# Optimization experiments

Hardware: AMD Instinct MI355X
Metric: run time of the kernel (lower is better)

## Reference

```python
import jax, jax.numpy as jnp
import numpy as np

B, N, K = 2, 8192, 16
D1, D2, OUT = 128, 256, 128


def setup_inputs() -> dict:
    key = jax.random.key(0)
    ks = jax.random.split(key, 6)
    return {
        "xyz1": jax.random.normal(ks[0], (B, N, 3), dtype=jnp.float32),
        "xyz2": jax.random.normal(ks[1], (B, N, 3), dtype=jnp.float32),
        "points1": jax.random.normal(ks[2], (B, N, D1), dtype=jnp.float32),
        "points2": jax.random.normal(ks[3], (B, N, D2), dtype=jnp.float32),
        # Conv1d(k=1) == pointwise linear: weight [OUT, D1+D2], bias [OUT]
        "W": jax.random.normal(ks[4], (OUT, D1 + D2), dtype=jnp.float32) / np.sqrt(D1 + D2).astype(np.float32),
        "b": jax.random.normal(ks[5], (OUT,), dtype=jnp.float32) * 0.01,
        "nsample": K,
    }


def reference(xyz1, xyz2, points1, points2, W, b, nsample):
    Bb, Nn, _ = xyz1.shape
    # squared pairwise distances, queries=xyz2, keys=xyz1 -> [B, N, N]
    d2 = (jnp.sum(xyz2 * xyz2, -1)[:, :, None]
          + jnp.sum(xyz1 * xyz1, -1)[:, None, :]
          - 2.0 * jnp.einsum('bsc,bnc->bsn', xyz2, xyz1))
    neg_vals, idx = jax.lax.top_k(-d2, nsample)          # K nearest
    dists = -neg_vals                                     # [B, N, K] sq dists
    recip = 1.0 / (dists + 1e-8)
    weight = recip / jnp.sum(recip, axis=2, keepdims=True)  # inverse-dist weights
    # gather neighbor features from points2: [B, N, K, D2]
    g = jnp.take_along_axis(points2, idx.reshape(Bb, Nn * nsample)[:, :, None], axis=1)
    g = g.reshape(Bb, Nn, nsample, -1)
    interp = jnp.sum(g * weight[..., None], axis=2)       # [B, N, D2]
    cat = jnp.concatenate([points1, interp], axis=-1)     # [B, N, D1+D2]
    # Conv1d(kernel=1) over channel dim
    return jnp.einsum('bnc,oc->bno', cat, W) + b
```

## Files before the change

kernel.cpp:

```cpp
#include <hip/hip_runtime.h>
#include <stdint.h>

#define BQ   2
#define NQ   8192
#define D1Q  128
#define D2Q  256
#define OUTQ 128
#define CATQ 384
#define KQ   16

#define NBIN 4096
#define RED_MARGIN 1e-3f
#define LB_MARGIN  1e-2f

#define WREG 3152

#define WS_WFH   0
#define WS_WFL   98304
#define WS_SPXYZ 262144
#define WS_QSXYZ 524288
#define WS_SPIDX 786432
#define WS_QSIDX 819200
#define WS_GBLO  851968
#define WS_GBHI  856064

__device__ __forceinline__ ushort f2bf(float f) {
    uint32_t u = __float_as_uint(f);
    return (ushort)((u + 0x7FFFu + ((u >> 16) & 1u)) >> 16);
}
__device__ __forceinline__ float bf2f(ushort h) {
    return __uint_as_float((uint32_t)h << 16);
}

__device__ __forceinline__ uint32_t encf(float f) {
    uint32_t b = __float_as_uint(f);
    return b ^ (0x80000000u | (uint32_t)((int32_t)b >> 31));
}
__device__ __forceinline__ float decf(uint32_t u) {
    uint32_t bits = (u & 0x80000000u) ? (u ^ 0x80000000u) : ~u;
    return __uint_as_float(bits);
}

__device__ __forceinline__ uint32_t mbcnt64(uint64_t m) {
    return __builtin_amdgcn_mbcnt_hi((uint32_t)(m >> 32),
           __builtin_amdgcn_mbcnt_lo((uint32_t)m, 0u));
}

typedef __attribute__((ext_vector_type(8))) short short8v;
typedef __attribute__((ext_vector_type(4))) float f32x4v;

__device__ __forceinline__ int mort_bin(float x, float y, float z) {
    int bx = (int)((x + 5.0f) * 1.6f); bx = bx < 0 ? 0 : (bx > 15 ? 15 : bx);
    int by = (int)((y + 5.0f) * 1.6f); by = by < 0 ? 0 : (by > 15 ? 15 : by);
    int bz = (int)((z + 5.0f) * 1.6f); bz = bz < 0 ? 0 : (bz > 15 ? 15 : bz);
    int k = 0;
    #pragma unroll
    for (int t = 0; t < 4; ++t)
        k |= (((bx >> t) & 1) << (3 * t)) | (((by >> t) & 1) << (3 * t + 1)) |
             (((bz >> t) & 1) << (3 * t + 2));
    return k;
}

__global__ __launch_bounds__(1024) void prep_all_kernel(
        const float* __restrict__ W,
        ushort* __restrict__ Wfh, ushort* __restrict__ Wfl,
        const float* __restrict__ xyz1, const float* __restrict__ xyz2,
        float4* __restrict__ sp_xyzn, float4* __restrict__ qs_xyzw,
        ushort* __restrict__ sp_idx, ushort* __restrict__ qs_idx,
        float4* __restrict__ gblo, float4* __restrict__ gbhi) {
    __shared__ uint32_t hist[NBIN];
    __shared__ uint32_t sc[16];
    __shared__ uint32_t ab[128 * 8];

    const int bid = blockIdx.x;
    const int tid = threadIdx.x;

    if (bid >= 4) {
        int flat = (bid - 4) * 1024 + tid;
        if (flat < CATQ * OUTQ) {
            int r    = flat & 7;
            int lane = (flat >> 3) & 63;
            int ctk  = flat >> 9;
            int ct   = ctk & 7;
            int kt   = ctk >> 3;
            int o = ct * 16 + (lane & 15);
            int k = kt * 32 + (lane >> 4) * 8 + r;
            float v  = W[o * CATQ + k];
            ushort h = f2bf(v);
            Wfh[flat] = h;
            Wfl[flat] = f2bf(v - bf2f(h));
        }
        return;
    }

    const int  batch = bid & 1;
    const bool isPts = bid < 2;
    const float* src = (isPts ? xyz1 : xyz2) + (size_t)batch * NQ * 3;

    #pragma unroll
    for (int i = tid; i < NBIN; i += 1024) hist[i] = 0u;
    if (isPts) ab[tid] = ((tid & 7) >= 4) ? 0u : 0xFFFFFFFFu;
    __syncthreads();

    float x[8], y[8], z[8];
    int   bin[8];
    #pragma unroll
    for (int e = 0; e < 8; ++e) {
        int idx = e * 1024 + tid;
        const float* p = src + (size_t)idx * 3;
        x[e] = p[0]; y[e] = p[1]; z[e] = p[2];
        bin[e] = mort_bin(x[e], y[e], z[e]);
        atomicAdd(&hist[bin[e]], 1u);
    }
    __syncthreads();

    uint32_t v0 = hist[4 * tid], v1 = hist[4 * tid + 1],
             v2 = hist[4 * tid + 2], v3 = hist[4 * tid + 3];
    uint32_t s = v0 + v1 + v2 + v3;
    uint32_t incl = s;
    #pragma unroll
    for (int d = 1; d < 64; d <<= 1) {
        uint32_t t = __shfl_up(incl, d, 64);
        if ((tid & 63) >= d) incl += t;
    }
    if ((tid & 63) == 63) sc[tid >> 6] = incl;
    __syncthreads();
    if (tid < 16) {
        uint32_t v = sc[tid];
        uint32_t i2 = v;
        #pragma unroll
        for (int d = 1; d < 16; d <<= 1) {
            uint32_t t = __shfl_up(i2, d, 64);
            if (tid >= d) i2 += t;
        }
        sc[tid] = i2 - v;
    }
    __syncthreads();
    uint32_t excl = sc[tid >> 6] + (incl - s);
    hist[4 * tid]     = excl;
    hist[4 * tid + 1] = excl + v0;
    hist[4 * tid + 2] = excl + v0 + v1;
    hist[4 * tid + 3] = excl + v0 + v1 + v2;
    __syncthreads();

    #pragma unroll
    for (int e = 0; e < 8; ++e) {
        int idx = e * 1024 + tid;
        uint32_t pos = atomicAdd(&hist[bin[e]], 1u);
        float n;
        {
            #pragma clang fp contract(off)
            float px = x[e] * x[e], py = y[e] * y[e], pz = z[e] * z[e];
            n = (px + py) + pz;
        }
        if (isPts) {
            sp_xyzn[batch * NQ + pos] = make_float4(x[e], y[e], z[e], n);
            sp_idx[batch * NQ + pos]  = (ushort)idx;
            uint32_t* gw = ab + ((pos >> 6) << 3);
            atomicMin(&gw[0], encf(x[e]));
            atomicMin(&gw[1], encf(y[e]));
            atomicMin(&gw[2], encf(z[e]));
            atomicMax(&gw[4], encf(x[e]));
            atomicMax(&gw[5], encf(y[e]));
            atomicMax(&gw[6], encf(z[e]));
        } else {
            qs_xyzw[batch * NQ + pos] = make_float4(x[e], y[e], z[e], n);
            qs_idx[batch * NQ + pos]  = (ushort)idx;
        }
    }
    if (isPts) {
        __syncthreads();
        if (tid < 128) {
            gblo[batch * 128 + tid] = make_float4(
                decf(ab[tid * 8 + 0]), decf(ab[tid * 8 + 1]),
                decf(ab[tid * 8 + 2]), 0.f);
            gbhi[batch * 128 + tid] = make_float4(
                decf(ab[tid * 8 + 4]), decf(ab[tid * 8 + 5]),
                decf(ab[tid * 8 + 6]), 0.f);
        }
    }
}

__device__ __forceinline__ float npy_d2(float4 pt, float qx, float qy, float qz,
                                        float s2) {
    #pragma clang fp contract(off)
    float d0  = pt.x * qx;
    float dot = fmaf(pt.y, qy, d0);
    dot       = fmaf(pt.z, qz, dot);
    float tt  = s2 + pt.w;
    return tt - 2.0f * dot;
}

__device__ __forceinline__ float red_r(float4 pt, float qx, float qy, float qz) {
    float dot = fmaf(pt.z, qz, fmaf(pt.y, qy, pt.x * qx));
    return fmaf(-2.0f, dot, pt.w);
}

__device__ __forceinline__ uint64_t sort64(uint64_t x, int lane) {
    #pragma unroll
    for (int k = 2; k <= 64; k <<= 1) {
        #pragma unroll
        for (int j = k >> 1; j > 0; j >>= 1) {
            uint64_t p = __shfl_xor((unsigned long long)x, j, 64);
            bool keep_min = (((lane & j) == 0) == ((lane & k) == 0));
            bool pless    = p < x;
            x = (pless == keep_min) ? p : x;
        }
    }
    return x;
}

__global__ __launch_bounds__(512, 8) void fused_kernel(
        const float4* __restrict__ sp_xyzn, const ushort* __restrict__ sp_idx,
        const float4* __restrict__ qs_xyzw, const ushort* __restrict__ qs_idx,
        const float* __restrict__ points1, const float* __restrict__ points2,
        const ushort* __restrict__ Wfh, const ushort* __restrict__ Wfl,
        const float* __restrict__ bias,
        const float4* __restrict__ gblo, const float4* __restrict__ gbhi,
        float* __restrict__ out) {
    __shared__ __align__(16) char smem[8 * WREG + 32];
    ushort* qsl = (ushort*)(smem + 8 * WREG);

    const int tid   = threadIdx.x;
    const int lane  = tid & 63;
    const int w     = tid >> 6;
    const int blk   = (blockIdx.x & 7) * 128 + (blockIdx.x >> 3);
    const int b     = blk >> 9;
    const int qslot = (blk & 511) * 16;

    char*     myreg   = smem + w * WREG;
    uint64_t* wball_w = (uint64_t*)myreg;
    ushort*   sl      = (ushort*)(myreg + 2048);

    if (tid < 16) qsl[tid] = qs_idx[b * NQ + qslot + tid];

    float qx[2], qy[2], qz[2], s2[2];
    int   oqi[2];
    #pragma unroll
    for (int j = 0; j < 2; ++j) {
        float4 q = qs_xyzw[(size_t)b * NQ + qslot + w * 2 + j];
        qx[j] = q.x; qy[j] = q.y; qz[j] = q.z; s2[j] = q.w;
        oqi[j] = (int)qs_idx[b * NQ + qslot + w * 2 + j];
    }

    const float4* spb = sp_xyzn + (size_t)b * NQ;
    const ushort* spi = sp_idx  + (size_t)b * NQ;

    int wstart = qslot + 8 - 512;
    if (wstart < 0) wstart = 0;
    if (wstart > NQ - 1024) wstart = NQ - 1024;
    wstart &= ~63;
    const float4* win = spb + wstart;

    float mn[2];
    #pragma unroll
    for (int j = 0; j < 2; ++j) mn[j] = __uint_as_float(0x7F800000u);

    #pragma unroll 8
    for (int s = 0; s < 16; ++s) {
        float4 pt = win[s * 64 + lane];
        #pragma unroll
        for (int j = 0; j < 2; ++j)
            mn[j] = fminf(mn[j], red_r(pt, qx[j], qy[j], qz[j]));
    }

    float that[2];
    #pragma unroll
    for (int j = 0; j < 2; ++j) {
        float x = mn[j];
        #pragma unroll
        for (int k = 2; k <= 64; k <<= 1) {
            #pragma unroll
            for (int jj = k >> 1; jj > 0; jj >>= 1) {
                float px = __shfl_xor(x, jj, 64);
                bool keep_min = (((lane & jj) == 0) == ((lane & k) == 0));
                float mnv = fminf(x, px), mxv = fmaxf(x, px);
                x = keep_min ? mnv : mxv;
            }
        }
        that[j] = s2[j] + __shfl(x, 15, 64) + RED_MARGIN;
    }

    int scnt_w = 0;
    {
        float qlx = fminf(qx[0], qx[1]);
        float qly = fminf(qy[0], qy[1]);
        float qlz = fminf(qz[0], qz[1]);
        float qhx = fmaxf(qx[0], qx[1]);
        float qhy = fmaxf(qy[0], qy[1]);
        float qhz = fmaxf(qz[0], qz[1]);
        float tmax = fmaxf(that[0], that[1]) + LB_MARGIN;
        #pragma unroll
        for (int h = 0; h < 2; ++h) {
            int g = h * 64 + lane;
            float4 gl = gblo[b * 128 + g];
            float4 gh = gbhi[b * 128 + g];
            float dx = fmaxf(fmaxf(qlx - gh.x, gl.x - qhx), 0.f);
            float dy = fmaxf(fmaxf(qly - gh.y, gl.y - qhy), 0.f);
            float dz = fmaxf(fmaxf(qlz - gh.z, gl.z - qhz), 0.f);
            float lb = dx * dx;
            lb = fmaf(dy, dy, lb);
            lb = fmaf(dz, dz, lb);
            bool sv = (lb <= tmax);
            uint64_t m = __ballot((int)sv);
            if (sv) sl[scnt_w + mbcnt64(m)] = (ushort)g;
            scnt_w += (int)__popcll(m);
        }
    }

    uint32_t cnt[2] = {0u, 0u};
    {
        float4 ptA = make_float4(0.f, 0.f, 0.f, 0.f), ptB = ptA;
        uint32_t pA = 0u, pB = 0u;
        if (scnt_w > 0) {
            int g = (int)sl[0];
            ptA = spb[g * 64 + lane]; pA = (uint32_t)spi[g * 64 + lane];
        }
        if (scnt_w > 1) {
            int g = (int)sl[1];
            ptB = spb[g * 64 + lane]; pB = (uint32_t)spi[g * 64 + lane];
        }
        for (int i = 0; i < scnt_w; ++i) {
            float4   pt   = ptA;
            uint32_t pidx = pA;
            ptA = ptB; pA = pB;
            if (i + 2 < scnt_w) {
                int g = (int)sl[i + 2];
                ptB = spb[g * 64 + lane];
                pB  = (uint32_t)spi[g * 64 + lane];
            }
            #pragma unroll
            for (int j = 0; j < 2; ++j) {
                float d2 = npy_d2(pt, qx[j], qy[j], qz[j], s2[j]);
                bool  v  = (d2 <= that[j]);
                uint64_t mask = __ballot((int)v);
                if (mask != 0ull) {
                    if (v) {
                        uint32_t pos    = cnt[j] + mbcnt64(mask);
                        uint32_t bits   = __float_as_uint(d2);
                        uint32_t mapped = bits ^ (0x80000000u |
                                          (uint32_t)((int32_t)bits >> 31));
                        if (pos < 128u)
                            wball_w[j * 128 + pos] =
                                ((uint64_t)mapped << 32) | (uint64_t)pidx;
                    }
                    cnt[j] += (uint32_t)__popcll(mask);
                }
            }
        }
    }

    int   myidxA[2];
    float mywgtA[2];
    #pragma unroll
    for (int j = 0; j < 2; ++j) {
        const uint64_t* wb = wball_w + (size_t)j * 128;
        const uint32_t c = cnt[j];
        uint64_t mykey;
        if (c <= 64u) {
            uint64_t k0 = (lane < (int)c) ? wb[lane] : ~0ull;
            mykey = sort64(k0, lane);
        } else {
            uint32_t cc = c > 128u ? 128u : c;
            uint64_t k0 = wb[lane];
            uint64_t k1 = (lane + 64 < (int)cc) ? wb[lane + 64] : ~0ull;
            k0 = sort64(k0, lane);
            k1 = sort64(k1, lane);
            uint64_t t1 = __shfl((unsigned long long)k1, lane & 15, 64);
            uint64_t km = (lane < 16) ? k0 : ((lane < 32) ? t1 : ~0ull);
            mykey = sort64(km, lane);
        }
        uint32_t mhi   = (uint32_t)(mykey >> 32);
        uint32_t rbits = (mhi & 0x80000000u) ? (mhi ^ 0x80000000u) : ~mhi;
        float    d2w   = __uint_as_float(rbits);
        myidxA[j] = (int)(uint32_t)(mykey & 0xFFFFFFFFull);
        float recip = (lane < KQ) ? (1.0f / (d2w + 1e-8f)) : 0.0f;
        float tot = recip;
        #pragma unroll
        for (int sh = 1; sh < 16; sh <<= 1) tot += __shfl_xor(tot, sh, 64);
        mywgtA[j] = recip / tot;
    }


    ushort* ch = (ushort*)myreg;
    ushort* cl = (ushort*)(myreg + 1568);
    const float* p2b = points2 + (size_t)b * NQ * D2Q;
    #pragma unroll
    for (int j = 0; j < 2; ++j) {
        if (lane < 32) {
            float4 p = ((const float4*)(points1 +
                        (size_t)(b * NQ + oqi[j]) * D1Q))[lane];
            ushort4 hv, lv;
            hv.x = f2bf(p.x); lv.x = f2bf(p.x - bf2f(hv.x));
            hv.y = f2bf(p.y); lv.y = f2bf(p.y - bf2f(hv.y));
            hv.z = f2bf(p.z); lv.z = f2bf(p.z - bf2f(hv.z));
            hv.w = f2bf(p.w); lv.w = f2bf(p.w - bf2f(hv.w));
            *(ushort4*)&ch[j * 392 + lane * 4] = hv;
            *(ushort4*)&cl[j * 392 + lane * 4] = lv;
        }
        float4 acc = make_float4(0.f, 0.f, 0.f, 0.f);
        #pragma unroll
        for (int k = 0; k < KQ; ++k) {
            int   kk = __builtin_amdgcn_readlane(myidxA[j], k);
            float wk = __uint_as_float((uint32_t)__builtin_amdgcn_readlane(
                           (int)__float_as_uint(mywgtA[j]), k));
            float4 row = ((const float4*)(p2b + (size_t)kk * D2Q))[lane];
            acc.x = fmaf(wk, row.x, acc.x);
            acc.y = fmaf(wk, row.y, acc.y);
            acc.z = fmaf(wk, row.z, acc.z);
            acc.w = fmaf(wk, row.w, acc.w);
        }
        {
            ushort4 hv, lv;
            hv.x = f2bf(acc.x); lv.x = f2bf(acc.x - bf2f(hv.x));
            hv.y = f2bf(acc.y); lv.y = f2bf(acc.y - bf2f(hv.y));
            hv.z = f2bf(acc.z); lv.z = f2bf(acc.z - bf2f(hv.z));
            hv.w = f2bf(acc.w); lv.w = f2bf(acc.w - bf2f(hv.w));
            *(ushort4*)&ch[j * 392 + D1Q + lane * 4] = hv;
            *(ushort4*)&cl[j * 392 + D1Q + lane * 4] = lv;
        }
    }
    __syncthreads();

    {
        const int arow = lane & 15;
        const int koff = (lane >> 4) * 8;
        const int ct   = w;
        const char* rowb = smem + (arow >> 1) * WREG + (arow & 1) * 784;
        f32x4v acc0 = {0.f, 0.f, 0.f, 0.f};
        #pragma unroll 4
        for (int kt = 0; kt < 12; ++kt) {
            short8v ah = *(const short8v*)(rowb + (kt * 32 + koff) * 2);
            short8v al = *(const short8v*)(rowb + 1568 + (kt * 32 + koff) * 2);
            const ushort* bhp = Wfh + ((size_t)(kt * 8 + ct) * 64 + lane) * 8;
            const ushort* blp = Wfl + ((size_t)(kt * 8 + ct) * 64 + lane) * 8;
            short8v bh0 = *(const short8v*)bhp;
            short8v bl0 = *(const short8v*)blp;
            acc0 = __builtin_amdgcn_mfma_f32_16x16x32_bf16(ah, bh0, acc0, 0, 0, 0);
            acc0 = __builtin_amdgcn_mfma_f32_16x16x32_bf16(al, bh0, acc0, 0, 0, 0);
            acc0 = __builtin_amdgcn_mfma_f32_16x16x32_bf16(ah, bl0, acc0, 0, 0, 0);
        }
        const int col0   = ct * 16 + (lane & 15);
        const int r0slot = (lane >> 4) * 4;
        const float bv0 = bias[col0];
        #pragma unroll
        for (int r = 0; r < 4; ++r) {
            int oq = (int)qsl[r0slot + r];
            size_t rowoff = (size_t)(b * NQ + oq) * OUTQ;
            out[rowoff + col0] = acc0[r] + bv0;
        }
    }
}

extern "C" void kernel_launch(void* const* d_in, const int* in_sizes, int n_in,
                              void* d_out, int out_size, void* d_ws, size_t ws_size,
                              hipStream_t stream) {
    const float* xyz1    = (const float*)d_in[0];
    const float* xyz2    = (const float*)d_in[1];
    const float* points1 = (const float*)d_in[2];
    const float* points2 = (const float*)d_in[3];
    const float* W       = (const float*)d_in[4];
    const float* bias    = (const float*)d_in[5];

    char* ws = (char*)d_ws;
    ushort*   Wfh     = (ushort*)(ws + WS_WFH);
    ushort*   Wfl     = (ushort*)(ws + WS_WFL);
    float4*   sp_xyzn = (float4*)(ws + WS_SPXYZ);
    float4*   qs_xyzw = (float4*)(ws + WS_QSXYZ);
    ushort*   sp_idx  = (ushort*)(ws + WS_SPIDX);
    ushort*   qs_idx  = (ushort*)(ws + WS_QSIDX);
    float4*   gblo    = (float4*)(ws + WS_GBLO);
    float4*   gbhi    = (float4*)(ws + WS_GBHI);

    prep_all_kernel<<<52, 1024, 0, stream>>>(W, Wfh, Wfl, xyz1, xyz2,
                                             sp_xyzn, qs_xyzw, sp_idx, qs_idx,
                                             gblo, gbhi);
    fused_kernel<<<(BQ * NQ) / 16, 512, 0, stream>>>(
        sp_xyzn, sp_idx, qs_xyzw, qs_idx, points1, points2,
        Wfh, Wfl, bias, gblo, gbhi, (float*)d_out);
}
```

Measured before the change: 150.6 us.

## Compute group bounding boxes via wave shuffles and deepen point prefetch to four

```diff
diff --git a/kernel.cpp b/kernel.cpp
--- a/kernel.cpp
+++ b/kernel.cpp
@@ -30,15 +30,6 @@
 }
 __device__ __forceinline__ float bf2f(ushort h) {
     return __uint_as_float((uint32_t)h << 16);
-}
-
-__device__ __forceinline__ uint32_t encf(float f) {
-    uint32_t b = __float_as_uint(f);
-    return b ^ (0x80000000u | (uint32_t)((int32_t)b >> 31));
-}
-__device__ __forceinline__ float decf(uint32_t u) {
-    uint32_t bits = (u & 0x80000000u) ? (u ^ 0x80000000u) : ~u;
-    return __uint_as_float(bits);
 }
 
 __device__ __forceinline__ uint32_t mbcnt64(uint64_t m) {
@@ -70,7 +61,6 @@
         float4* __restrict__ gblo, float4* __restrict__ gbhi) {
     __shared__ uint32_t hist[NBIN];
     __shared__ uint32_t sc[16];
-    __shared__ uint32_t ab[128 * 8];
 
     const int bid = blockIdx.x;
     const int tid = threadIdx.x;
@@ -99,7 +89,6 @@
 
     #pragma unroll
     for (int i = tid; i < NBIN; i += 1024) hist[i] = 0u;
-    if (isPts) ab[tid] = ((tid & 7) >= 4) ? 0u : 0xFFFFFFFFu;
     __syncthreads();
 
     float x[8], y[8], z[8];
@@ -156,27 +145,35 @@
         if (isPts) {
             sp_xyzn[batch * NQ + pos] = make_float4(x[e], y[e], z[e], n);
             sp_idx[batch * NQ + pos]  = (ushort)idx;
-            uint32_t* gw = ab + ((pos >> 6) << 3);
-            atomicMin(&gw[0], encf(x[e]));
-            atomicMin(&gw[1], encf(y[e]));
-            atomicMin(&gw[2], encf(z[e]));
-            atomicMax(&gw[4], encf(x[e]));
-            atomicMax(&gw[5], encf(y[e]));
-            atomicMax(&gw[6], encf(z[e]));
         } else {
             qs_xyzw[batch * NQ + pos] = make_float4(x[e], y[e], z[e], n);
             qs_idx[batch * NQ + pos]  = (ushort)idx;
         }
     }
+
     if (isPts) {
         __syncthreads();
-        if (tid < 128) {
-            gblo[batch * 128 + tid] = make_float4(
-                decf(ab[tid * 8 + 0]), decf(ab[tid * 8 + 1]),
-                decf(ab[tid * 8 + 2]), 0.f);
-            gbhi[batch * 128 + tid] = make_float4(
-                decf(ab[tid * 8 + 4]), decf(ab[tid * 8 + 5]),
-                decf(ab[tid * 8 + 6]), 0.f);
+        const int wv   = tid >> 6;
+        const int lane = tid & 63;
+        #pragma unroll
+        for (int k = 0; k < 8; ++k) {
+            int g = wv * 8 + k;
+            float4 pt = sp_xyzn[(size_t)batch * NQ + g * 64 + lane];
+            float lx = pt.x, ly = pt.y, lz = pt.z;
+            float hx = pt.x, hy = pt.y, hz = pt.z;
+            #pragma unroll
+            for (int d = 1; d < 64; d <<= 1) {
+                lx = fminf(lx, __shfl_xor(lx, d, 64));
+                ly = fminf(ly, __shfl_xor(ly, d, 64));
+                lz = fminf(lz, __shfl_xor(lz, d, 64));
+                hx = fmaxf(hx, __shfl_xor(hx, d, 64));
+                hy = fmaxf(hy, __shfl_xor(hy, d, 64));
+                hz = fmaxf(hz, __shfl_xor(hz, d, 64));
+            }
+            if (lane == 0) {
+                gblo[batch * 128 + g] = make_float4(lx, ly, lz, 0.f);
+                gbhi[batch * 128 + g] = make_float4(hx, hy, hz, 0.f);
+            }
         }
     }
 }
@@ -310,8 +307,9 @@
 
     uint32_t cnt[2] = {0u, 0u};
     {
-        float4 ptA = make_float4(0.f, 0.f, 0.f, 0.f), ptB = ptA;
-        uint32_t pA = 0u, pB = 0u;
+        float4 ptA = make_float4(0.f, 0.f, 0.f, 0.f);
+        float4 ptB = ptA, ptC = ptA, ptD = ptA;
+        uint32_t pA = 0u, pB = 0u, pC = 0u, pD = 0u;
         if (scnt_w > 0) {
             int g = (int)sl[0];
             ptA = spb[g * 64 + lane]; pA = (uint32_t)spi[g * 64 + lane];
@@ -319,15 +317,25 @@
         if (scnt_w > 1) {
             int g = (int)sl[1];
             ptB = spb[g * 64 + lane]; pB = (uint32_t)spi[g * 64 + lane];
+        }
+        if (scnt_w > 2) {
+            int g = (int)sl[2];
+            ptC = spb[g * 64 + lane]; pC = (uint32_t)spi[g * 64 + lane];
+        }
+        if (scnt_w > 3) {
+            int g = (int)sl[3];
+            ptD = spb[g * 64 + lane]; pD = (uint32_t)spi[g * 64 + lane];
         }
         for (int i = 0; i < scnt_w; ++i) {
             float4   pt   = ptA;
             uint32_t pidx = pA;
             ptA = ptB; pA = pB;
-            if (i + 2 < scnt_w) {
-                int g = (int)sl[i + 2];
-                ptB = spb[g * 64 + lane];
-                pB  = (uint32_t)spi[g * 64 + lane];
+            ptB = ptC; pB = pC;
+            ptC = ptD; pC = pD;
+            if (i + 4 < scnt_w) {
+                int g = (int)sl[i + 4];
+                ptD = spb[g * 64 + lane];
+                pD  = (uint32_t)spi[g * 64 + lane];
             }
             #pragma unroll
             for (int j = 0; j < 2; ++j) {
```

Result: slower. 160.6 us (+6.7%).
